# Optimization experiments

Measured on AMD Instinct MI355X. Metric: run time of the kernel, lower is better.

The kernel has to match this reference:

```python
import jax, jax.numpy as jnp
import numpy as np

ALPHA = 1.702
LIMIT = 7.0
EPS = 1e-5

E, K, H, I = 8, 2, 2048, 2048
B, S = 1, 1024


def setup_inputs() -> dict:
    key = jax.random.key(0)
    k1, k2, k3, k4, k5 = jax.random.split(key, 5)
    x = jax.random.normal(k1, (B, S, H), dtype=jnp.float32)
    norm_w = jax.random.normal(k2, (H,), dtype=jnp.float32) * 0.02 + 1.0
    router_w = jax.random.normal(k3, (E, H), dtype=jnp.float32) * (1.0 / np.sqrt(H))
    w_gu = jax.random.normal(k4, (E, H, 2 * I), dtype=jnp.float32) * (1.0 / np.sqrt(H))
    w_down = jax.random.normal(k5, (E, I, H), dtype=jnp.float32) * (1.0 / np.sqrt(I))
    return {"x": x, "norm_w": norm_w, "router_w": router_w,
            "w_gu": w_gu, "w_down": w_down, "top_k": K}


def _rmsnorm(x, w):
    var = jnp.mean(x * x, axis=-1, keepdims=True)
    return x * jax.lax.rsqrt(var + EPS) * w


def _swiglu(h):
    # interleaved gate/linear halves, clamped (GPT-OSS style)
    glu = jnp.minimum(h[..., ::2], LIMIT)
    lin = jnp.clip(h[..., 1::2], -LIMIT, LIMIT)
    return glu * jax.nn.sigmoid(ALPHA * glu) * (lin + 1.0)


def reference(x, norm_w, router_w, w_gu, w_down, top_k):
    b, s, h = x.shape
    t = _rmsnorm(x, norm_w).reshape(b * s, h)          # [T, H]
    T = t.shape[0]

    # Router: linear -> softmax -> top-k -> normalize selected affinities
    logits = jnp.einsum('th,eh->te', t, router_w)      # [T, E]
    probs = jax.nn.softmax(logits, axis=-1)
    vals, idx = jax.lax.top_k(probs, top_k)            # [T, K]
    vals = vals / jnp.sum(vals, axis=-1, keepdims=True)
    cw = jnp.zeros_like(probs).at[jnp.arange(T)[:, None], idx].add(vals)  # [T, E]

    # Expert MLPs (dense per-expert reference of the blockwise grouped GEMM)
    hgu = jnp.einsum('th,ehf->etf', t, w_gu)           # [E, T, 2I]
    act = _swiglu(hgu)                                 # [E, T, I]
    oe = jnp.einsum('eti,eio->eto', act, w_down)       # [E, T, H]
    out = jnp.einsum('eto,te->to', oe, cw)             # [T, H]
    return out.reshape(b, s, h)
```

## Files before the change

kernel.cpp:

```cpp
#include <hip/hip_runtime.h>
#include <hip/hip_bf16.h>

#define H_   2048
#define E_   8
#define T_   1024
#define TWOI 4096
#define I_   2048
#define ALPHA 1.702f
#define LIMIT 7.0f

#define BM 128
#define BN 128
#define BKK 32
#define BTW 40

typedef __attribute__((ext_vector_type(8))) short short8;
typedef __attribute__((ext_vector_type(4))) float f32x4;

#define AS3U(p) ((__attribute__((address_space(3))) unsigned int*)(p))
#define AS1U(p) ((const __attribute__((address_space(1))) unsigned int*)(p))

__device__ __forceinline__ unsigned short f2bf(float f) {
    unsigned int u = __float_as_uint(f);
    u += 0x7fff + ((u >> 16) & 1);
    return (unsigned short)(u >> 16);
}

__device__ __forceinline__ unsigned int cvtpk_bf16(float lo, float hi) {
    unsigned int r;
    asm("v_cvt_pk_bf16_f32 %0, %1, %2" : "=v"(r) : "v"(lo), "v"(hi));
    return r;
}

__global__ void zero_counts(int* __restrict__ counts) {
    int i = threadIdx.x;
    if (i < E_) counts[i] = 0;
}

__global__ __launch_bounds__(256) void rms_router(
    const float* __restrict__ x, const float* __restrict__ nw,
    const float* __restrict__ rw,
    unsigned short* __restrict__ tbf, int* __restrict__ counts,
    int* __restrict__ tlist, int* __restrict__ tslot, float* __restrict__ tw)
{
    int t = blockIdx.x;
    int tid = threadIdx.x;
    int wave = tid >> 6, lane = tid & 63;
    const float* xr = x + (size_t)t * H_;

    float4 v0 = *(const float4*)(xr + tid * 4);
    float4 v1 = *(const float4*)(xr + 1024 + tid * 4);
    float ss = v0.x*v0.x + v0.y*v0.y + v0.z*v0.z + v0.w*v0.w
             + v1.x*v1.x + v1.y*v1.y + v1.z*v1.z + v1.w*v1.w;
    #pragma unroll
    for (int s = 32; s; s >>= 1) ss += __shfl_xor(ss, s);

    __shared__ float red[4];
    __shared__ float wlog[4][8];
    if (lane == 0) red[wave] = ss;
    __syncthreads();
    float total = red[0] + red[1] + red[2] + red[3];
    float scale = rsqrtf(total * (1.0f / H_) + 1e-5f);

    float4 n0 = *(const float4*)(nw + tid * 4);
    float4 n1 = *(const float4*)(nw + 1024 + tid * 4);
    float tv[8];
    tv[0] = v0.x * scale * n0.x; tv[1] = v0.y * scale * n0.y;
    tv[2] = v0.z * scale * n0.z; tv[3] = v0.w * scale * n0.w;
    tv[4] = v1.x * scale * n1.x; tv[5] = v1.y * scale * n1.y;
    tv[6] = v1.z * scale * n1.z; tv[7] = v1.w * scale * n1.w;

    ushort4 o0 = make_ushort4(f2bf(tv[0]), f2bf(tv[1]), f2bf(tv[2]), f2bf(tv[3]));
    ushort4 o1 = make_ushort4(f2bf(tv[4]), f2bf(tv[5]), f2bf(tv[6]), f2bf(tv[7]));
    *(ushort4*)(tbf + (size_t)t * H_ + tid * 4) = o0;
    *(ushort4*)(tbf + (size_t)t * H_ + 1024 + tid * 4) = o1;

    float acc[E_];
    #pragma unroll
    for (int e = 0; e < E_; e++) {
        const float* r0 = rw + (size_t)e * H_ + tid * 4;
        float4 a = *(const float4*)r0;
        float4 b = *(const float4*)(r0 + 1024);
        acc[e] = tv[0]*a.x + tv[1]*a.y + tv[2]*a.z + tv[3]*a.w
               + tv[4]*b.x + tv[5]*b.y + tv[6]*b.z + tv[7]*b.w;
    }
    #pragma unroll
    for (int s = 32; s; s >>= 1)
        #pragma unroll
        for (int e = 0; e < E_; e++) acc[e] += __shfl_xor(acc[e], s);
    if (lane == 0)
        #pragma unroll
        for (int e = 0; e < E_; e++) wlog[wave][e] = acc[e];
    __syncthreads();

    if (tid == 0) {
        float lg[E_];
        #pragma unroll
        for (int e = 0; e < E_; e++)
            lg[e] = wlog[0][e] + wlog[1][e] + wlog[2][e] + wlog[3][e];
        int i0 = 0;
        #pragma unroll
        for (int e = 1; e < E_; e++) if (lg[e] > lg[i0]) i0 = e;
        int i1 = -1;
        #pragma unroll
        for (int e = 0; e < E_; e++) {
            if (e == i0) continue;
            if (i1 < 0 || lg[e] > lg[i1]) i1 = e;
        }
        float e1 = expf(lg[i1] - lg[i0]);
        float s = 1.0f + e1;
        float w0 = 1.0f / s, w1 = e1 / s;
        int p0 = atomicAdd(&counts[i0], 1);
        tlist[i0 * T_ + p0] = t; tslot[i0 * T_ + p0] = 0; tw[i0 * T_ + p0] = w0;
        int p1 = atomicAdd(&counts[i1], 1);
        tlist[i1 * T_ + p1] = t; tslot[i1 * T_ + p1] = 1; tw[i1 * T_ + p1] = w1;
    }
}

__device__ __forceinline__ void compute_step(
    const unsigned short (*Asb)[BKK], const unsigned short (*Btb)[BTW],
    int wm, int wn, int lane, f32x4 acc[4][4])
{
    short8 a[4], b[4];
    int arow = wm * 64 + (lane & 15);
    int brow = wn * 64 + (lane & 15);
    int koff = (lane >> 4) * 8;
    #pragma unroll
    for (int mi = 0; mi < 4; mi++)
        a[mi] = *(const short8*)(&Asb[arow + mi * 16][koff]);
    #pragma unroll
    for (int ni = 0; ni < 4; ni++)
        b[ni] = *(const short8*)(&Btb[brow + ni * 16][koff]);
    #pragma unroll
    for (int mi = 0; mi < 4; mi++)
        #pragma unroll
        for (int ni = 0; ni < 4; ni++)
            acc[mi][ni] = __builtin_amdgcn_mfma_f32_16x16x32_bf16(a[mi], b[ni], acc[mi][ni], 0, 0, 0);
}

#define STEP(TT, RCUR, RNEXT, PRE) {                                               \
    if (PRE) {                                                                     \
        int kk2_ = ((TT) + 2) * BKK;                                               \
        __builtin_amdgcn_global_load_lds(AS1U(asrc0 + kk2_), AS3U(&As[c2][wave * 32][0]), 16, 0, 0);      \
        __builtin_amdgcn_global_load_lds(AS1U(asrc1 + kk2_), AS3U(&As[c2][wave * 32 + 16][0]), 16, 0, 0); \
        _Pragma("unroll")                                                          \
        for (int j = 0; j < 16; j++)                                               \
            RNEXT[j] = bcol[(size_t)(kk2_ + sk + j) * ldbv];                       \
    }                                                                              \
    compute_step(As[c0], Bt[(TT) & 1], wm, wn, lane, acc);                         \
    {                                                                              \
        unsigned int pk_[8];                                                       \
        _Pragma("unroll")                                                          \
        for (int h = 0; h < 8; h++) pk_[h] = cvtpk_bf16(RCUR[2 * h], RCUR[2 * h + 1]); \
        unsigned short* db_ = &Bt[((TT) + 1) & 1][sn][sk];                         \
        *(uint4*)(db_)     = make_uint4(pk_[0], pk_[1], pk_[2], pk_[3]);           \
        *(uint4*)(db_ + 8) = make_uint4(pk_[4], pk_[5], pk_[6], pk_[7]);           \
    }                                                                              \
    if (PRE) { asm volatile("s_waitcnt vmcnt(18)" ::: "memory"); }                 \
    else     { asm volatile("s_waitcnt vmcnt(0)"  ::: "memory"); }                 \
    asm volatile("s_waitcnt lgkmcnt(0)" ::: "memory");                             \
    __builtin_amdgcn_sched_barrier(0);                                             \
    __builtin_amdgcn_s_barrier();                                                  \
    __builtin_amdgcn_sched_barrier(0);                                             \
    { int tmp_ = c0; c0 = c1; c1 = c2; c2 = tmp_; }                                \
}

#define GEMM_PIPELINE(NS)                                                          \
    float r0[16], r1[16];                                                          \
    int c0 = 0, c1 = 1, c2 = 2;                                                    \
                                    \
    __builtin_amdgcn_global_load_lds(AS1U(asrc0), AS3U(&As[0][wave * 32][0]), 16, 0, 0);            \
    __builtin_amdgcn_global_load_lds(AS1U(asrc1), AS3U(&As[0][wave * 32 + 16][0]), 16, 0, 0);       \
    _Pragma("unroll")                                                              \
    for (int j = 0; j < 16; j++) r0[j] = bcol[(size_t)(sk + j) * ldbv];            \
    __builtin_amdgcn_global_load_lds(AS1U(asrc0 + BKK), AS3U(&As[1][wave * 32][0]), 16, 0, 0);      \
    __builtin_amdgcn_global_load_lds(AS1U(asrc1 + BKK), AS3U(&As[1][wave * 32 + 16][0]), 16, 0, 0); \
    _Pragma("unroll")                                                              \
    for (int j = 0; j < 16; j++) r1[j] = bcol[(size_t)(BKK + sk + j) * ldbv];      \
    {                                                                              \
        unsigned int pk_[8];                                                       \
        _Pragma("unroll")                                                          \
        for (int h = 0; h < 8; h++) pk_[h] = cvtpk_bf16(r0[2 * h], r0[2 * h + 1]); \
        unsigned short* db_ = &Bt[0][sn][sk];                                      \
        *(uint4*)(db_)     = make_uint4(pk_[0], pk_[1], pk_[2], pk_[3]);           \
        *(uint4*)(db_ + 8) = make_uint4(pk_[4], pk_[5], pk_[6], pk_[7]);           \
    }                                                                              \
    asm volatile("s_waitcnt vmcnt(18)" ::: "memory");                              \
    asm volatile("s_waitcnt lgkmcnt(0)" ::: "memory");                             \
    __builtin_amdgcn_sched_barrier(0);                                             \
    __builtin_amdgcn_s_barrier();                                                  \
    __builtin_amdgcn_sched_barrier(0);                                             \
    for (int t = 0; t < (NS) - 2; t += 2) {                                        \
        STEP(t,     r1, r0, 1)                                                     \
        STEP(t + 1, r0, r1, 1)                                                     \
    }                                                                              \
    STEP((NS) - 2, r1, r0, 0)                                                      \
    compute_step(As[c0], Bt[((NS) - 1) & 1], wm, wn, lane, acc);

__global__ __launch_bounds__(256, 3) void gu_gemm(
    const unsigned short* __restrict__ tbf,
    const float* __restrict__ wgu,
    const int* __restrict__ counts, const int* __restrict__ tlist,
    unsigned short* __restrict__ act)
{
    int bid = blockIdx.x;
    int mtile = bid >> 8;
    int rem = bid & 255;
    int e = rem >> 5;
    int n0 = (rem & 31) * BN;

    int cnt = counts[e];
    int m0 = mtile * BM;
    if (m0 >= cnt) return;

    __shared__ __align__(16) unsigned short As[3][BM][BKK];
    __shared__ __align__(16) unsigned short Bt[2][BN][BTW];

    int tid = threadIdx.x;
    int lane = tid & 63, wave = tid >> 6;
    int wm = wave >> 1, wn = wave & 1;

    int row0 = wave * 32 + (lane >> 2);
    int gr0 = m0 + row0, gr1 = gr0 + 16;
    int tok0 = tlist[e * T_ + (gr0 < cnt ? gr0 : 0)];
    int tok1 = tlist[e * T_ + (gr1 < cnt ? gr1 : 0)];
    const unsigned short* asrc0 = tbf + (size_t)tok0 * H_ + (lane & 3) * 8;
    const unsigned short* asrc1 = tbf + (size_t)tok1 * H_ + (lane & 3) * 8;

    int sn = tid & 127;
    int sk = (tid >> 7) * 16;
    const float* bcol = wgu + (size_t)e * H_ * TWOI + n0 + sn;
    const int ldbv = TWOI;

    f32x4 acc[4][4];
    #pragma unroll
    for (int mi = 0; mi < 4; mi++)
        #pragma unroll
        for (int ni = 0; ni < 4; ni++) acc[mi][ni] = (f32x4){0.f, 0.f, 0.f, 0.f};

    GEMM_PIPELINE(64)

    #pragma unroll
    for (int mi = 0; mi < 4; mi++) {
        #pragma unroll
        for (int ni = 0; ni < 4; ni++) {
            #pragma unroll
            for (int r = 0; r < 4; r++) {
                float v = acc[mi][ni][r];
                float p = __shfl_xor(v, 1);
                int rowe = wm * 64 + mi * 16 + (lane >> 4) * 4 + r;
                int grow = m0 + rowe;
                if (!(lane & 1) && grow < cnt) {
                    float glu = fminf(v, LIMIT);
                    float lin = fminf(fmaxf(p, -LIMIT), LIMIT);
                    float g = glu / (1.0f + __expf(-ALPHA * glu));
                    float a_ = g * (lin + 1.0f);
                    int col = n0 + wn * 64 + ni * 16 + (lane & 15);
                    act[((size_t)e * T_ + grow) * I_ + (col >> 1)] = f2bf(a_);
                }
            }
        }
    }
}

__global__ __launch_bounds__(256, 3) void down_gemm(
    const unsigned short* __restrict__ act,
    const float* __restrict__ wdn,
    const int* __restrict__ counts, const int* __restrict__ tlist,
    const int* __restrict__ tslot, const float* __restrict__ tw,
    float* __restrict__ parts)
{
    int bid = blockIdx.x;
    int mtile = bid >> 8;
    int rem = bid & 255;
    int e = rem >> 5;
    int ks = (rem >> 4) & 1;
    int ntile = rem & 15;
    int n0 = ntile * BN;
    int kbase = ks * (I_ / 2);

    int cnt = counts[e];
    int m0 = mtile * BM;
    if (m0 >= cnt) return;

    __shared__ __align__(16) unsigned short As[3][BM][BKK];
    __shared__ __align__(16) unsigned short Bt[2][BN][BTW];

    int tid = threadIdx.x;
    int lane = tid & 63, wave = tid >> 6;
    int wm = wave >> 1, wn = wave & 1;

    int row0 = wave * 32 + (lane >> 2);
    const unsigned short* asrc0 = act + ((size_t)e * T_ + m0 + row0) * I_ + kbase + (lane & 3) * 8;
    const unsigned short* asrc1 = asrc0 + (size_t)16 * I_;

    int sn = tid & 127;
    int sk = (tid >> 7) * 16;
    const float* bcol = wdn + (size_t)e * I_ * H_ + (size_t)kbase * H_ + n0 + sn;
    const int ldbv = H_;

    f32x4 acc[4][4];
    #pragma unroll
    for (int mi = 0; mi < 4; mi++)
        #pragma unroll
        for (int ni = 0; ni < 4; ni++) acc[mi][ni] = (f32x4){0.f, 0.f, 0.f, 0.f};

    GEMM_PIPELINE(32)

    #pragma unroll
    for (int mi = 0; mi < 4; mi++) {
        int rowe = wm * 64 + mi * 16 + (lane >> 4) * 4;
        int grow0 = m0 + rowe;
        #pragma unroll
        for (int r = 0; r < 4; r++) {
            int grow = grow0 + r;
            if (grow < cnt) {
                int tok  = tlist[e * T_ + grow];
                int slot = tslot[e * T_ + grow];
                float w  = tw[e * T_ + grow];
                float* dst = parts + ((size_t)(ks * 2 + slot) * T_ + tok) * H_;
                #pragma unroll
                for (int ni = 0; ni < 4; ni++) {
                    int col = n0 + wn * 64 + ni * 16 + (lane & 15);
                    dst[col] = w * acc[mi][ni][r];
                }
            }
        }
    }
}

__global__ __launch_bounds__(256) void combine_kernel(
    const float* __restrict__ parts, float* __restrict__ out)
{
    int i = blockIdx.x * blockDim.x + threadIdx.x;
    const float4* p0 = (const float4*)parts;
    const float4* p1 = (const float4*)(parts + (size_t)T_ * H_);
    const float4* p2 = (const float4*)(parts + (size_t)2 * T_ * H_);
    const float4* p3 = (const float4*)(parts + (size_t)3 * T_ * H_);
    float4 a = p0[i], b = p1[i], c = p2[i], d = p3[i];
    float4 s;
    s.x = (a.x + b.x) + (c.x + d.x);
    s.y = (a.y + b.y) + (c.y + d.y);
    s.z = (a.z + b.z) + (c.z + d.z);
    s.w = (a.w + b.w) + (c.w + d.w);
    ((float4*)out)[i] = s;
}

extern "C" void kernel_launch(void* const* d_in, const int* in_sizes, int n_in,
                              void* d_out, int out_size, void* d_ws, size_t ws_size,
                              hipStream_t stream)
{
    const float* x   = (const float*)d_in[0];
    const float* nw  = (const float*)d_in[1];
    const float* rw  = (const float*)d_in[2];
    const float* wgu = (const float*)d_in[3];
    const float* wdn = (const float*)d_in[4];
    float* out = (float*)d_out;

    char* ws = (char*)d_ws;
    unsigned short* tbf = (unsigned short*)ws;
    unsigned short* act = (unsigned short*)(ws + (4u << 20));
    float* parts = (float*)(ws + (36u << 20));
    int*   counts = (int*)(ws + (68u << 20));
    int*   tlist  = (int*)(ws + (68u << 20) + 256);
    int*   tslot  = (int*)(ws + (68u << 20) + 256 + 32 * 1024);
    float* tw     = (float*)(ws + (68u << 20) + 256 + 64 * 1024);

    zero_counts<<<dim3(1), 64, 0, stream>>>(counts);
    rms_router<<<dim3(T_), 256, 0, stream>>>(x, nw, rw, tbf, counts, tlist, tslot, tw);
    gu_gemm<<<dim3(2048), 256, 0, stream>>>(tbf, wgu, counts, tlist, act);
    down_gemm<<<dim3(2048), 256, 0, stream>>>(act, wdn, counts, tlist, tslot, tw, parts);
    combine_kernel<<<dim3((T_ * H_ / 4) / 256), 256, 0, stream>>>(parts, out);
}
```

Measured before the change: 189.3 us.

## Load A operand fragments directly from global into registers, dropping LDS staging

The A operand (token activations) is no longer staged through a triple-buffered LDS tile via global_load_lds. Each lane now loads its MFMA A fragments straight from global memory into registers one k-step ahead, and the explicit vmcnt waits are removed. This cuts LDS traffic and shared-memory footprint, which could allow more resident blocks. In exchange each A row is loaded redundantly by the two waves that share wm, and the global load latency is exposed to the compute step with less buffering.

After: 243.5 us. +28.6%, slower.

```diff
diff --git a/kernel.cpp b/kernel.cpp
--- a/kernel.cpp
+++ b/kernel.cpp
@@ -16,9 +16,6 @@
 
 typedef __attribute__((ext_vector_type(8))) short short8;
 typedef __attribute__((ext_vector_type(4))) float f32x4;
-
-#define AS3U(p) ((__attribute__((address_space(3))) unsigned int*)(p))
-#define AS1U(p) ((const __attribute__((address_space(1))) unsigned int*)(p))
 
 __device__ __forceinline__ unsigned short f2bf(float f) {
     unsigned int u = __float_as_uint(f);
@@ -118,17 +115,13 @@
 }
 
 __device__ __forceinline__ void compute_step(
-    const unsigned short (*Asb)[BKK], const unsigned short (*Btb)[BTW],
-    int wm, int wn, int lane, f32x4 acc[4][4])
-{
-    short8 a[4], b[4];
-    int arow = wm * 64 + (lane & 15);
+    const short8 a[4], const unsigned short (*Btb)[BTW],
+    int wn, int lane, f32x4 acc[4][4])
+{
+    short8 b[4];
     int brow = wn * 64 + (lane & 15);
     int koff = (lane >> 4) * 8;
     #pragma unroll
-    for (int mi = 0; mi < 4; mi++)
-        a[mi] = *(const short8*)(&Asb[arow + mi * 16][koff]);
-    #pragma unroll
     for (int ni = 0; ni < 4; ni++)
         b[ni] = *(const short8*)(&Btb[brow + ni * 16][koff]);
     #pragma unroll
@@ -138,17 +131,24 @@
             acc[mi][ni] = __builtin_amdgcn_mfma_f32_16x16x32_bf16(a[mi], b[ni], acc[mi][ni], 0, 0, 0);
 }
 
-#define STEP(TT, RCUR, RNEXT, PRE) {                                               \
-    if (PRE) {                                                                     \
+#define STEP(TT, ACUR, ANXT, RCUR, RNXT, MODE) {                                   \
+    if ((MODE) == 2) {                                                             \
+        int kk1_ = ((TT) + 1) * BKK;                                               \
+        _Pragma("unroll")                                                          \
+        for (int mi = 0; mi < 4; mi++)                                             \
+            ANXT[mi] = *(const short8*)(ap[mi] + kk1_);                            \
         int kk2_ = ((TT) + 2) * BKK;                                               \
-        __builtin_amdgcn_global_load_lds(AS1U(asrc0 + kk2_), AS3U(&As[c2][wave * 32][0]), 16, 0, 0);      \
-        __builtin_amdgcn_global_load_lds(AS1U(asrc1 + kk2_), AS3U(&As[c2][wave * 32 + 16][0]), 16, 0, 0); \
         _Pragma("unroll")                                                          \
         for (int j = 0; j < 16; j++)                                               \
-            RNEXT[j] = bcol[(size_t)(kk2_ + sk + j) * ldbv];                       \
-    }                                                                              \
-    compute_step(As[c0], Bt[(TT) & 1], wm, wn, lane, acc);                         \
-    {                                                                              \
+            RNXT[j] = bcol[(size_t)(kk2_ + sk + j) * ldbv];                        \
+    } else if ((MODE) == 1) {                                                      \
+        int kk1_ = ((TT) + 1) * BKK;                                               \
+        _Pragma("unroll")                                                          \
+        for (int mi = 0; mi < 4; mi++)                                             \
+            ANXT[mi] = *(const short8*)(ap[mi] + kk1_);                            \
+    }                                                                              \
+    __builtin_amdgcn_sched_barrier(0);                                             \
+    if ((MODE) >= 1) {                                                             \
         unsigned int pk_[8];                                                       \
         _Pragma("unroll")                                                          \
         for (int h = 0; h < 8; h++) pk_[h] = cvtpk_bf16(RCUR[2 * h], RCUR[2 * h + 1]); \
@@ -156,46 +156,44 @@
         *(uint4*)(db_)     = make_uint4(pk_[0], pk_[1], pk_[2], pk_[3]);           \
         *(uint4*)(db_ + 8) = make_uint4(pk_[4], pk_[5], pk_[6], pk_[7]);           \
     }                                                                              \
-    if (PRE) { asm volatile("s_waitcnt vmcnt(18)" ::: "memory"); }                 \
-    else     { asm volatile("s_waitcnt vmcnt(0)"  ::: "memory"); }                 \
-    asm volatile("s_waitcnt lgkmcnt(0)" ::: "memory");                             \
+    compute_step(ACUR, Bt[(TT) & 1], wn, lane, acc);                               \
+    if ((MODE) >= 1) {                                                             \
+        asm volatile("s_waitcnt lgkmcnt(0)" ::: "memory");                         \
+        __builtin_amdgcn_sched_barrier(0);                                         \
+        __builtin_amdgcn_s_barrier();                                              \
+        __builtin_amdgcn_sched_barrier(0);                                         \
+    }                                                                              \
+}
+
+#define GEMM_PIPELINE(NS)                                                          \
+    short8 aA[4], aB[4];                                                           \
+    float rA[16], rB[16];                                                          \
+                            \
+    _Pragma("unroll")                                                              \
+    for (int mi = 0; mi < 4; mi++) aA[mi] = *(const short8*)(ap[mi]);              \
+    _Pragma("unroll")                                                              \
+    for (int j = 0; j < 16; j++) rA[j] = bcol[(size_t)(sk + j) * ldbv];            \
+    _Pragma("unroll")                                                              \
+    for (int j = 0; j < 16; j++) rB[j] = bcol[(size_t)(BKK + sk + j) * ldbv];      \
     __builtin_amdgcn_sched_barrier(0);                                             \
-    __builtin_amdgcn_s_barrier();                                                  \
-    __builtin_amdgcn_sched_barrier(0);                                             \
-    { int tmp_ = c0; c0 = c1; c1 = c2; c2 = tmp_; }                                \
-}
-
-#define GEMM_PIPELINE(NS)                                                          \
-    float r0[16], r1[16];                                                          \
-    int c0 = 0, c1 = 1, c2 = 2;                                                    \
-                                    \
-    __builtin_amdgcn_global_load_lds(AS1U(asrc0), AS3U(&As[0][wave * 32][0]), 16, 0, 0);            \
-    __builtin_amdgcn_global_load_lds(AS1U(asrc1), AS3U(&As[0][wave * 32 + 16][0]), 16, 0, 0);       \
-    _Pragma("unroll")                                                              \
-    for (int j = 0; j < 16; j++) r0[j] = bcol[(size_t)(sk + j) * ldbv];            \
-    __builtin_amdgcn_global_load_lds(AS1U(asrc0 + BKK), AS3U(&As[1][wave * 32][0]), 16, 0, 0);      \
-    __builtin_amdgcn_global_load_lds(AS1U(asrc1 + BKK), AS3U(&As[1][wave * 32 + 16][0]), 16, 0, 0); \
-    _Pragma("unroll")                                                              \
-    for (int j = 0; j < 16; j++) r1[j] = bcol[(size_t)(BKK + sk + j) * ldbv];      \
     {                                                                              \
         unsigned int pk_[8];                                                       \
         _Pragma("unroll")                                                          \
-        for (int h = 0; h < 8; h++) pk_[h] = cvtpk_bf16(r0[2 * h], r0[2 * h + 1]); \
+        for (int h = 0; h < 8; h++) pk_[h] = cvtpk_bf16(rA[2 * h], rA[2 * h + 1]); \
         unsigned short* db_ = &Bt[0][sn][sk];                                      \
         *(uint4*)(db_)     = make_uint4(pk_[0], pk_[1], pk_[2], pk_[3]);           \
         *(uint4*)(db_ + 8) = make_uint4(pk_[4], pk_[5], pk_[6], pk_[7]);           \
     }                                                                              \
-    asm volatile("s_waitcnt vmcnt(18)" ::: "memory");                              \
     asm volatile("s_waitcnt lgkmcnt(0)" ::: "memory");                             \
     __builtin_amdgcn_sched_barrier(0);                                             \
     __builtin_amdgcn_s_barrier();                                                  \
     __builtin_amdgcn_sched_barrier(0);                                             \
     for (int t = 0; t < (NS) - 2; t += 2) {                                        \
-        STEP(t,     r1, r0, 1)                                                     \
-        STEP(t + 1, r0, r1, 1)                                                     \
-    }                                                                              \
-    STEP((NS) - 2, r1, r0, 0)                                                      \
-    compute_step(As[c0], Bt[((NS) - 1) & 1], wm, wn, lane, acc);
+        STEP(t,     aA, aB, rB, rA, 2)                                             \
+        STEP(t + 1, aB, aA, rA, rB, 2)                                             \
+    }                                                                              \
+    STEP((NS) - 2, aA, aB, rB, rA, 1)                                              \
+    STEP((NS) - 1, aB, aA, rA, rB, 0)
 
 __global__ __launch_bounds__(256, 3) void gu_gemm(
     const unsigned short* __restrict__ tbf,
@@ -213,19 +211,21 @@
     int m0 = mtile * BM;
     if (m0 >= cnt) return;
 
-    __shared__ __align__(16) unsigned short As[3][BM][BKK];
     __shared__ __align__(16) unsigned short Bt[2][BN][BTW];
 
     int tid = threadIdx.x;
     int lane = tid & 63, wave = tid >> 6;
     int wm = wave >> 1, wn = wave & 1;
 
-    int row0 = wave * 32 + (lane >> 2);
-    int gr0 = m0 + row0, gr1 = gr0 + 16;
-    int tok0 = tlist[e * T_ + (gr0 < cnt ? gr0 : 0)];
-    int tok1 = tlist[e * T_ + (gr1 < cnt ? gr1 : 0)];
-    const unsigned short* asrc0 = tbf + (size_t)tok0 * H_ + (lane & 3) * 8;
-    const unsigned short* asrc1 = tbf + (size_t)tok1 * H_ + (lane & 3) * 8;
+    int arow = m0 + wm * 64 + (lane & 15);
+    int koffel = (lane >> 4) * 8;
+    const unsigned short* ap[4];
+    #pragma unroll
+    for (int mi = 0; mi < 4; mi++) {
+        int gr = arow + mi * 16;
+        int tok = tlist[e * T_ + (gr < cnt ? gr : 0)];
+        ap[mi] = tbf + (size_t)tok * H_ + koffel;
+    }
 
     int sn = tid & 127;
     int sk = (tid >> 7) * 16;
@@ -283,16 +283,18 @@
     int m0 = mtile * BM;
     if (m0 >= cnt) return;
 
-    __shared__ __align__(16) unsigned short As[3][BM][BKK];
     __shared__ __align__(16) unsigned short Bt[2][BN][BTW];
 
     int tid = threadIdx.x;
     int lane = tid & 63, wave = tid >> 6;
     int wm = wave >> 1, wn = wave & 1;
 
-    int row0 = wave * 32 + (lane >> 2);
-    const unsigned short* asrc0 = act + ((size_t)e * T_ + m0 + row0) * I_ + kbase + (lane & 3) * 8;
-    const unsigned short* asrc1 = asrc0 + (size_t)16 * I_;
+    int arow = m0 + wm * 64 + (lane & 15);
+    int koffel = (lane >> 4) * 8;
+    const unsigned short* ap[4];
+    #pragma unroll
+    for (int mi = 0; mi < 4; mi++)
+        ap[mi] = act + ((size_t)e * T_ + arow + mi * 16) * I_ + kbase + koffel;
 
     int sn = tid & 127;
     int sk = (tid >> 7) * 16;
```

## Stage A tiles through registers with double-buffered LDS instead of direct global-to-LDS loads

Applied to the files above, without the earlier changes.

Replaces the async global_load_lds path for the activation (A) operand with plain vector loads into registers that are written to LDS after each compute step, alongside the existing B staging. This drops the A LDS buffer from triple to double buffering and the waits on vector-memory counters, and raises the launch-bounds occupancy hint from 3 to 4 blocks per CU. It aims for more resident waves to hide load latency, at the cost of extra VGPRs for the staged A data and extra LDS write instructions per step.

Result: slower. 534.8 us (+182.4%).

```diff
diff --git a/kernel.cpp b/kernel.cpp
--- a/kernel.cpp
+++ b/kernel.cpp
@@ -16,9 +16,6 @@
 
 typedef __attribute__((ext_vector_type(8))) short short8;
 typedef __attribute__((ext_vector_type(4))) float f32x4;
-
-#define AS3U(p) ((__attribute__((address_space(3))) unsigned int*)(p))
-#define AS1U(p) ((const __attribute__((address_space(1))) unsigned int*)(p))
 
 __device__ __forceinline__ unsigned short f2bf(float f) {
     unsigned int u = __float_as_uint(f);
@@ -138,66 +135,70 @@
             acc[mi][ni] = __builtin_amdgcn_mfma_f32_16x16x32_bf16(a[mi], b[ni], acc[mi][ni], 0, 0, 0);
 }
 
-#define STEP(TT, RCUR, RNEXT, PRE) {                                               \
-    if (PRE) {                                                                     \
+#define STEP(TT, AC0, AC1, AN0, AN1, RCUR, RNXT, MODE) {                           \
+    if ((MODE) == 2) {                                                             \
         int kk2_ = ((TT) + 2) * BKK;                                               \
-        __builtin_amdgcn_global_load_lds(AS1U(asrc0 + kk2_), AS3U(&As[c2][wave * 32][0]), 16, 0, 0);      \
-        __builtin_amdgcn_global_load_lds(AS1U(asrc1 + kk2_), AS3U(&As[c2][wave * 32 + 16][0]), 16, 0, 0); \
+        AN0 = *(const uint4*)(asrc0 + kk2_);                                       \
+        AN1 = *(const uint4*)(asrc1 + kk2_);                                       \
         _Pragma("unroll")                                                          \
         for (int j = 0; j < 16; j++)                                               \
-            RNEXT[j] = bcol[(size_t)(kk2_ + sk + j) * ldbv];                       \
+            RNXT[j] = bcol[(size_t)(kk2_ + sk + j) * ldbv];                        \
     }                                                                              \
-    compute_step(As[c0], Bt[(TT) & 1], wm, wn, lane, acc);                         \
-    {                                                                              \
+    __builtin_amdgcn_sched_barrier(0);                                             \
+    compute_step(As[(TT) & 1], Bt[(TT) & 1], wm, wn, lane, acc);                   \
+    if ((MODE) >= 1) {                                                             \
         unsigned int pk_[8];                                                       \
         _Pragma("unroll")                                                          \
         for (int h = 0; h < 8; h++) pk_[h] = cvtpk_bf16(RCUR[2 * h], RCUR[2 * h + 1]); \
         unsigned short* db_ = &Bt[((TT) + 1) & 1][sn][sk];                         \
         *(uint4*)(db_)     = make_uint4(pk_[0], pk_[1], pk_[2], pk_[3]);           \
         *(uint4*)(db_ + 8) = make_uint4(pk_[4], pk_[5], pk_[6], pk_[7]);           \
+        unsigned short* da_ = &As[((TT) + 1) & 1][wave * 32 + (lane >> 2)][(lane & 3) * 8]; \
+        *(uint4*)(da_)       = AC0;                                                \
+        *(uint4*)(da_ + 512) = AC1;                    \
+        asm volatile("s_waitcnt lgkmcnt(0)" ::: "memory");                         \
+        __builtin_amdgcn_sched_barrier(0);                                         \
+        __builtin_amdgcn_s_barrier();                                              \
+        __builtin_amdgcn_sched_barrier(0);                                         \
     }                                                                              \
-    if (PRE) { asm volatile("s_waitcnt vmcnt(18)" ::: "memory"); }                 \
-    else     { asm volatile("s_waitcnt vmcnt(0)"  ::: "memory"); }                 \
-    asm volatile("s_waitcnt lgkmcnt(0)" ::: "memory");                             \
+}
+
+#define GEMM_PIPELINE(NS)                                                          \
+    uint4 aA0, aA1, aB0, aB1;                                                      \
+    float rA[16], rB[16];                                                          \
+               \
+    aA0 = *(const uint4*)(asrc0);                                                  \
+    aA1 = *(const uint4*)(asrc1);                                                  \
+    _Pragma("unroll")                                                              \
+    for (int j = 0; j < 16; j++) rA[j] = bcol[(size_t)(sk + j) * ldbv];            \
+    aB0 = *(const uint4*)(asrc0 + BKK);                                            \
+    aB1 = *(const uint4*)(asrc1 + BKK);                                            \
+    _Pragma("unroll")                                                              \
+    for (int j = 0; j < 16; j++) rB[j] = bcol[(size_t)(BKK + sk + j) * ldbv];      \
     __builtin_amdgcn_sched_barrier(0);                                             \
-    __builtin_amdgcn_s_barrier();                                                  \
-    __builtin_amdgcn_sched_barrier(0);                                             \
-    { int tmp_ = c0; c0 = c1; c1 = c2; c2 = tmp_; }                                \
-}
-
-#define GEMM_PIPELINE(NS)                                                          \
-    float r0[16], r1[16];                                                          \
-    int c0 = 0, c1 = 1, c2 = 2;                                                    \
-                                    \
-    __builtin_amdgcn_global_load_lds(AS1U(asrc0), AS3U(&As[0][wave * 32][0]), 16, 0, 0);            \
-    __builtin_amdgcn_global_load_lds(AS1U(asrc1), AS3U(&As[0][wave * 32 + 16][0]), 16, 0, 0);       \
-    _Pragma("unroll")                                                              \
-    for (int j = 0; j < 16; j++) r0[j] = bcol[(size_t)(sk + j) * ldbv];            \
-    __builtin_amdgcn_global_load_lds(AS1U(asrc0 + BKK), AS3U(&As[1][wave * 32][0]), 16, 0, 0);      \
-    __builtin_amdgcn_global_load_lds(AS1U(asrc1 + BKK), AS3U(&As[1][wave * 32 + 16][0]), 16, 0, 0); \
-    _Pragma("unroll")                                                              \
-    for (int j = 0; j < 16; j++) r1[j] = bcol[(size_t)(BKK + sk + j) * ldbv];      \
     {                                                                              \
         unsigned int pk_[8];                                                       \
         _Pragma("unroll")                                                          \
-        for (int h = 0; h < 8; h++) pk_[h] = cvtpk_bf16(r0[2 * h], r0[2 * h + 1]); \
+        for (int h = 0; h < 8; h++) pk_[h] = cvtpk_bf16(rA[2 * h], rA[2 * h + 1]); \
         unsigned short* db_ = &Bt[0][sn][sk];                                      \
         *(uint4*)(db_)     = make_uint4(pk_[0], pk_[1], pk_[2], pk_[3]);           \
         *(uint4*)(db_ + 8) = make_uint4(pk_[4], pk_[5], pk_[6], pk_[7]);           \
+        unsigned short* da_ = &As[0][wave * 32 + (lane >> 2)][(lane & 3) * 8];     \
+        *(uint4*)(da_)       = aA0;                                                \
+        *(uint4*)(da_ + 512) = aA1;                                                \
     }                                                                              \
-    asm volatile("s_waitcnt vmcnt(18)" ::: "memory");                              \
     asm volatile("s_waitcnt lgkmcnt(0)" ::: "memory");                             \
     __builtin_amdgcn_sched_barrier(0);                                             \
     __builtin_amdgcn_s_barrier();                                                  \
     __builtin_amdgcn_sched_barrier(0);                                             \
     for (int t = 0; t < (NS) - 2; t += 2) {                                        \
-        STEP(t,     r1, r0, 1)                                                     \
-        STEP(t + 1, r0, r1, 1)                                                     \
+        STEP(t,     aB0, aB1, aA0, aA1, rB, rA, 2)                                 \
+        STEP(t + 1, aA0, aA1, aB0, aB1, rA, rB, 2)                                 \
     }                                                                              \
-    STEP((NS) - 2, r1, r0, 0)                                                      \
-    compute_step(As[c0], Bt[((NS) - 1) & 1], wm, wn, lane, acc);
-
-__global__ __launch_bounds__(256, 3) void gu_gemm(
+    STEP((NS) - 2, aB0, aB1, aA0, aA1, rB, rA, 1)                                  \
+    STEP((NS) - 1, aA0, aA1, aB0, aB1, rA, rB, 0)
+
+__global__ __launch_bounds__(256, 4) void gu_gemm(
     const unsigned short* __restrict__ tbf,
     const float* __restrict__ wgu,
     const int* __restrict__ counts, const int* __restrict__ tlist,
@@ -213,7 +214,7 @@
     int m0 = mtile * BM;
     if (m0 >= cnt) return;
 
-    __shared__ __align__(16) unsigned short As[3][BM][BKK];
+    __shared__ __align__(16) unsigned short As[2][BM][BKK];
     __shared__ __align__(16) unsigned short Bt[2][BN][BTW];
 
     int tid = threadIdx.x;
@@ -263,7 +264,7 @@
     }
 }
 
-__global__ __launch_bounds__(256, 3) void down_gemm(
+__global__ __launch_bounds__(256, 4) void down_gemm(
     const unsigned short* __restrict__ act,
     const float* __restrict__ wdn,
     const int* __restrict__ counts, const int* __restrict__ tlist,
@@ -283,7 +284,7 @@
     int m0 = mtile * BM;
     if (m0 >= cnt) return;
 
-    __shared__ __align__(16) unsigned short As[3][BM][BKK];
+    __shared__ __align__(16) unsigned short As[2][BM][BKK];
     __shared__ __align__(16) unsigned short Bt[2][BN][BTW];
 
     int tid = threadIdx.x;
```

## Split gate/up GEMM along K and apply SwiGLU in separate reduction kernel

Applied to the files above, without the earlier changes.

The gate/up GEMM is split into two K halves, which doubles the grid to 4096 blocks. Each block writes fp32 partial sums to a new workspace buffer. A new swiglu_combine kernel adds the two partials, applies the clamped SwiGLU and writes bf16 activations. This aims for better occupancy across CUs, since token counts per expert are uneven and many M-tiles exit early. In exchange it adds a large fp32 intermediate write and read, about 256 MB of space, plus one extra launch.

After: 234.8 us. 24.0% more time.

```diff
diff --git a/kernel.cpp b/kernel.cpp
--- a/kernel.cpp
+++ b/kernel.cpp
@@ -201,13 +201,15 @@
     const unsigned short* __restrict__ tbf,
     const float* __restrict__ wgu,
     const int* __restrict__ counts, const int* __restrict__ tlist,
-    unsigned short* __restrict__ act)
+    float* __restrict__ hgu)
 {
     int bid = blockIdx.x;
-    int mtile = bid >> 8;
-    int rem = bid & 255;
-    int e = rem >> 5;
+    int mtile = bid >> 9;
+    int rem = bid & 511;
+    int e = rem >> 6;
+    int ks = (rem >> 5) & 1;
     int n0 = (rem & 31) * BN;
+    int kbase = ks * (H_ / 2);
 
     int cnt = counts[e];
     int m0 = mtile * BM;
@@ -224,12 +226,12 @@
     int gr0 = m0 + row0, gr1 = gr0 + 16;
     int tok0 = tlist[e * T_ + (gr0 < cnt ? gr0 : 0)];
     int tok1 = tlist[e * T_ + (gr1 < cnt ? gr1 : 0)];
-    const unsigned short* asrc0 = tbf + (size_t)tok0 * H_ + (lane & 3) * 8;
-    const unsigned short* asrc1 = tbf + (size_t)tok1 * H_ + (lane & 3) * 8;
+    const unsigned short* asrc0 = tbf + (size_t)tok0 * H_ + kbase + (lane & 3) * 8;
+    const unsigned short* asrc1 = tbf + (size_t)tok1 * H_ + kbase + (lane & 3) * 8;
 
     int sn = tid & 127;
     int sk = (tid >> 7) * 16;
-    const float* bcol = wgu + (size_t)e * H_ * TWOI + n0 + sn;
+    const float* bcol = wgu + (size_t)e * H_ * TWOI + (size_t)kbase * TWOI + n0 + sn;
     const int ldbv = TWOI;
 
     f32x4 acc[4][4];
@@ -238,29 +240,59 @@
         #pragma unroll
         for (int ni = 0; ni < 4; ni++) acc[mi][ni] = (f32x4){0.f, 0.f, 0.f, 0.f};
 
-    GEMM_PIPELINE(64)
-
+    GEMM_PIPELINE(32)
+
+    float* hbase = hgu + (size_t)ks * 8192 * TWOI;
     #pragma unroll
     for (int mi = 0; mi < 4; mi++) {
-        #pragma unroll
-        for (int ni = 0; ni < 4; ni++) {
-            #pragma unroll
-            for (int r = 0; r < 4; r++) {
-                float v = acc[mi][ni][r];
-                float p = __shfl_xor(v, 1);
-                int rowe = wm * 64 + mi * 16 + (lane >> 4) * 4 + r;
-                int grow = m0 + rowe;
-                if (!(lane & 1) && grow < cnt) {
-                    float glu = fminf(v, LIMIT);
-                    float lin = fminf(fmaxf(p, -LIMIT), LIMIT);
-                    float g = glu / (1.0f + __expf(-ALPHA * glu));
-                    float a_ = g * (lin + 1.0f);
+        int rowe = wm * 64 + mi * 16 + (lane >> 4) * 4;
+        int grow0 = m0 + rowe;
+        #pragma unroll
+        for (int r = 0; r < 4; r++) {
+            int grow = grow0 + r;
+            if (grow < cnt) {
+                float* dst = hbase + ((size_t)e * T_ + grow) * TWOI;
+                #pragma unroll
+                for (int ni = 0; ni < 4; ni++) {
                     int col = n0 + wn * 64 + ni * 16 + (lane & 15);
-                    act[((size_t)e * T_ + grow) * I_ + (col >> 1)] = f2bf(a_);
+                    dst[col] = acc[mi][ni][r];
                 }
             }
         }
     }
+}
+
+__global__ __launch_bounds__(256) void swiglu_combine(
+    const float* __restrict__ hgu, const int* __restrict__ counts,
+    unsigned short* __restrict__ act)
+{
+    int idx = blockIdx.x * blockDim.x + threadIdx.x;
+    int row = idx >> 9;
+    int c0 = (idx & 511) * 4;
+    int e = row >> 10;
+    int grow = row & 1023;
+    if (grow >= counts[e]) return;
+
+    const float* h0 = hgu + (size_t)row * TWOI + c0 * 2;
+    const float* h1 = h0 + (size_t)8192 * TWOI;
+    float4 a0 = *(const float4*)(h0);
+    float4 a1 = *(const float4*)(h0 + 4);
+    float4 b0 = *(const float4*)(h1);
+    float4 b1 = *(const float4*)(h1 + 4);
+
+    float hv[8];
+    hv[0] = a0.x + b0.x; hv[1] = a0.y + b0.y; hv[2] = a0.z + b0.z; hv[3] = a0.w + b0.w;
+    hv[4] = a1.x + b1.x; hv[5] = a1.y + b1.y; hv[6] = a1.z + b1.z; hv[7] = a1.w + b1.w;
+
+    unsigned short o[4];
+    #pragma unroll
+    for (int j = 0; j < 4; j++) {
+        float glu = fminf(hv[2 * j], LIMIT);
+        float lin = fminf(fmaxf(hv[2 * j + 1], -LIMIT), LIMIT);
+        float g = glu / (1.0f + __expf(-ALPHA * glu));
+        o[j] = f2bf(g * (lin + 1.0f));
+    }
+    *(ushort4*)(act + (size_t)row * I_ + c0) = make_ushort4(o[0], o[1], o[2], o[3]);
 }
 
 __global__ __launch_bounds__(256, 3) void down_gemm(
@@ -361,14 +393,16 @@
     unsigned short* tbf = (unsigned short*)ws;
     unsigned short* act = (unsigned short*)(ws + (4u << 20));
     float* parts = (float*)(ws + (36u << 20));
-    int*   counts = (int*)(ws + (68u << 20));
-    int*   tlist  = (int*)(ws + (68u << 20) + 256);
-    int*   tslot  = (int*)(ws + (68u << 20) + 256 + 32 * 1024);
-    float* tw     = (float*)(ws + (68u << 20) + 256 + 64 * 1024);
+    float* hgu   = (float*)(ws + (68u << 20));
+    int*   counts = (int*)(ws + (324u << 20));
+    int*   tlist  = (int*)(ws + (324u << 20) + 256);
+    int*   tslot  = (int*)(ws + (324u << 20) + 256 + 32 * 1024);
+    float* tw     = (float*)(ws + (324u << 20) + 256 + 64 * 1024);
 
     zero_counts<<<dim3(1), 64, 0, stream>>>(counts);
     rms_router<<<dim3(T_), 256, 0, stream>>>(x, nw, rw, tbf, counts, tlist, tslot, tw);
-    gu_gemm<<<dim3(2048), 256, 0, stream>>>(tbf, wgu, counts, tlist, act);
+    gu_gemm<<<dim3(4096), 256, 0, stream>>>(tbf, wgu, counts, tlist, hgu);
+    swiglu_combine<<<dim3(8192 * 512 / 256), 256, 0, stream>>>(hgu, counts, act);
     down_gemm<<<dim3(2048), 256, 0, stream>>>(act, wdn, counts, tlist, tslot, tw, parts);
     combine_kernel<<<dim3((T_ * H_ / 4) / 256), 256, 0, stream>>>(parts, out);
 }
```
